# Kernel optimization log

Measured on AMD Instinct MI355X. Metric: run time of the kernel, lower is better.

Reference implementation:

```python
import jax, jax.numpy as jnp
import numpy as np

R, C = 30, 56
N = R * C  # 1680
K = 0.005
PRCN = 15
ALPHA = 1.0
BETA = 1.0


def setup_inputs() -> dict:
    key = jax.random.key(0)
    k1, k2 = jax.random.split(key)
    net_in = jax.random.normal(k1, (2 * N,), dtype=jnp.float32)
    # Recurrent connectivity matrix (learned weight in the original, loaded from .mat)
    J = jax.random.normal(k2, (N, N), dtype=jnp.float32) / np.float32(np.sqrt(N))
    return {"net_in": net_in, "J": J}


def reference(net_in, J):
    Iext = net_in[:N].reshape(R, C)
    r0 = net_in[N:2 * N].reshape(R, C)

    def step(r, _):
        # 4-way chunked mm + cat in the original == single matvec J @ r_flat
        temp = (J @ r.reshape(N)).reshape(R, C)
        U = ALPHA * (BETA * temp) + ALPHA * Iext
        sq = jnp.square(0.2 * U)
        recSum = jnp.sum(K * sq)
        # (0.2*U)^2 * (0.04 / recSum) / 0.04  ==  sq / recSum, kept explicit for fidelity
        r_new = sq * (0.04 / recSum) / 0.04
        return r_new, (U, recSum)

    r_last, (Us, sums) = jax.lax.scan(step, r0, None, length=PRCN - 1)
    return Us[-1], sums[-1], r_last
```

## Files before the change

### kernel.cpp

```cpp
#include <hip/hip_runtime.h>


typedef float f32x4 __attribute__((ext_vector_type(4)));

#define N      1680
#define NV4    420
#define NSTEP  14
#define GBLK   105
#define RPB    16
#define RPW    4

__device__ __forceinline__ void jload7_issue(
    const f32x4* p0, const f32x4* p1, const f32x4* p2, const f32x4* p3,
    const f32x4* p4, const f32x4* p5, const f32x4* p6,
    f32x4& v0, f32x4& v1, f32x4& v2, f32x4& v3,
    f32x4& v4, f32x4& v5, f32x4& v6)
{
    asm volatile(
        "global_load_dwordx4 %0, %7, off\n\t"
        "global_load_dwordx4 %1, %8, off\n\t"
        "global_load_dwordx4 %2, %9, off\n\t"
        "global_load_dwordx4 %3, %10, off\n\t"
        "global_load_dwordx4 %4, %11, off\n\t"
        "global_load_dwordx4 %5, %12, off\n\t"
        "global_load_dwordx4 %6, %13, off"
        : "=&v"(v0), "=&v"(v1), "=&v"(v2), "=&v"(v3),
          "=&v"(v4), "=&v"(v5), "=&v"(v6)
        : "v"(p0), "v"(p1), "v"(p2), "v"(p3), "v"(p4), "v"(p5), "v"(p6));
}

__device__ __forceinline__ void vm_wait0() {
    asm volatile("s_waitcnt vmcnt(0)" ::: "memory");
    __builtin_amdgcn_sched_barrier(0);
}

__device__ __forceinline__ void load7_llc(
    const f32x4* p0, const f32x4* p1, const f32x4* p2, const f32x4* p3,
    const f32x4* p4, const f32x4* p5, const f32x4* p6,
    f32x4& v0, f32x4& v1, f32x4& v2, f32x4& v3,
    f32x4& v4, f32x4& v5, f32x4& v6)
{
    asm volatile(
        "global_load_dwordx4 %0, %7, off sc0 sc1\n\t"
        "global_load_dwordx4 %1, %8, off sc0 sc1\n\t"
        "global_load_dwordx4 %2, %9, off sc0 sc1\n\t"
        "global_load_dwordx4 %3, %10, off sc0 sc1\n\t"
        "global_load_dwordx4 %4, %11, off sc0 sc1\n\t"
        "global_load_dwordx4 %5, %12, off sc0 sc1\n\t"
        "global_load_dwordx4 %6, %13, off sc0 sc1\n\t"
        "s_waitcnt vmcnt(0)"
        : "=&v"(v0), "=&v"(v1), "=&v"(v2), "=&v"(v3),
          "=&v"(v4), "=&v"(v5), "=&v"(v6)
        : "v"(p0), "v"(p1), "v"(p2), "v"(p3), "v"(p4), "v"(p5), "v"(p6)
        : "memory");
}

__device__ __forceinline__ void llc_store4(f32x4* p, f32x4 v) {
    asm volatile("global_store_dwordx4 %0, %1, off sc0 sc1"
                 :: "v"(p), "v"(v) : "memory");
}

__global__ __launch_bounds__(256, 1) void fused_recur(
    const float* __restrict__ J,
    const float* __restrict__ net_in,
    float* __restrict__ out,
    float* __restrict__ ws)
{
    __shared__ f32x4 lds_r[2][NV4];
    __shared__ float lds_flag[16];

    f32x4* bufs = (f32x4*)ws;

    const int tid  = threadIdx.x;
    const int lane = tid & 63;
    const int wave = tid >> 6;
    const int row0 = (int)blockIdx.x * RPB + wave * RPW;

    const unsigned pend0 = (lane < 36) ? 0x7Fu : 0x3Fu;

    if (tid < 16) lds_flag[tid] = 0.0f;
    __syncthreads();

    float iext[RPW];
    #pragma unroll
    for (int m = 0; m < RPW; ++m) iext[m] = net_in[row0 + m];

    const f32x4* jb[RPW];
    #pragma unroll
    for (int m = 0; m < RPW; ++m)
        jb[m] = (const f32x4*)(J + (size_t)(row0 + m) * N);

    float Uv[RPW], Qv[RPW];

    #pragma unroll 1
    for (int t = 0; t < NSTEP; ++t) {
        f32x4 Jr[RPW][7];
        #pragma unroll
        for (int m = 0; m < RPW; ++m)
            jload7_issue(jb[m] + lane,       jb[m] + lane + 64,
                         jb[m] + lane + 128, jb[m] + lane + 192,
                         jb[m] + lane + 256, jb[m] + lane + 320,
                         (lane < 36) ? (jb[m] + lane + 384) : jb[m],
                         Jr[m][0], Jr[m][1], Jr[m][2], Jr[m][3],
                         Jr[m][4], Jr[m][5], Jr[m][6]);

        f32x4 rv[7];
        float psum = 0.0f;
        const int par = (t - 1) & 1;

        if (t == 0) {
            vm_wait0();
            const f32x4* r0 = (const f32x4*)(net_in + N);
            #pragma unroll
            for (int k = 0; k < 7; ++k) {
                const int idx = lane + 64 * k;
                rv[k] = (idx < NV4) ? r0[idx] : (f32x4)0.f;
            }
        } else if (wave == 0) {
            const f32x4* base = bufs + (size_t)(t - 1) * NV4;
            const f32x4* q0 = base + lane;
            const f32x4* q1 = base + lane + 64;
            const f32x4* q2 = base + lane + 128;
            const f32x4* q3 = base + lane + 192;
            const f32x4* q4 = base + lane + 256;
            const f32x4* q5 = base + lane + 320;
            const f32x4* q6 = (lane < 36) ? (base + lane + 384) : base;

            unsigned pend = pend0;
            #pragma unroll 1
            for (;;) {
                load7_llc(q0, q1, q2, q3, q4, q5, q6,
                          rv[0], rv[1], rv[2], rv[3], rv[4], rv[5], rv[6]);
                #pragma unroll
                for (int k = 0; k < 7; ++k) {
                    if ((pend >> k) & 1u) {
                        const f32x4 q = rv[k];
                        const float mn = fminf(fminf(q[0], q[1]),
                                               fminf(q[2], q[3]));
                        if (mn >= 0.0f) {
                            lds_r[par][lane + 64 * k] = q;
                            pend &= ~(1u << k);
                        }
                    }
                }
                if (!__any(pend != 0u)) break;
            }
            if (lane == 0)
                __hip_atomic_store(&lds_flag[t - 1], 1.0f, __ATOMIC_RELEASE,
                                   __HIP_MEMORY_SCOPE_WORKGROUP);
            if (lane >= 36) rv[6] = (f32x4)0.f;
            #pragma unroll
            for (int k = 0; k < 7; ++k)
                psum += (rv[k][0] + rv[k][1]) + (rv[k][2] + rv[k][3]);
        } else {
            while (__hip_atomic_load(&lds_flag[t - 1], __ATOMIC_ACQUIRE,
                                     __HIP_MEMORY_SCOPE_WORKGROUP) == 0.0f) {}
            vm_wait0();
            #pragma unroll
            for (int k = 0; k < 7; ++k) {
                const int idx = lane + 64 * k;
                rv[k] = (idx < NV4) ? lds_r[par][idx] : (f32x4)0.f;
            }
            #pragma unroll
            for (int k = 0; k < 7; ++k)
                psum += (rv[k][0] + rv[k][1]) + (rv[k][2] + rv[k][3]);
        }

        f32x4 acc[RPW];
        #pragma unroll
        for (int m = 0; m < RPW; ++m) acc[m] = (f32x4)0.f;
        #pragma unroll
        for (int k = 0; k < 7; ++k) {
            #pragma unroll
            for (int m = 0; m < RPW; ++m) {
                acc[m][0] += Jr[m][k][0] * rv[k][0];
                acc[m][1] += Jr[m][k][1] * rv[k][1];
                acc[m][2] += Jr[m][k][2] * rv[k][2];
                acc[m][3] += Jr[m][k][3] * rv[k][3];
            }
        }
        float red[5];
        #pragma unroll
        for (int m = 0; m < RPW; ++m)
            red[m] = (acc[m][0] + acc[m][1]) + (acc[m][2] + acc[m][3]);
        red[4] = psum;
        #pragma unroll
        for (int off = 32; off; off >>= 1) {
            #pragma unroll
            for (int i = 0; i < 5; ++i) red[i] += __shfl_xor(red[i], off, 64);
        }
        const float inv = (t == 0) ? 1.0f : 1.0f / (0.005f * red[4]);

        #pragma unroll
        for (int m = 0; m < RPW; ++m) {
            const float U  = red[m] * inv + iext[m];
            const float u2 = 0.2f * U;
            Uv[m] = U;
            Qv[m] = u2 * u2;
        }

        if (lane == 0) {
            f32x4 pub = { Qv[0], Qv[1], Qv[2], Qv[3] };
            llc_store4(bufs + (size_t)t * NV4 + (row0 >> 2), pub);
        }
    }

    float s13;
    if (wave == 0) {
        const f32x4* base = bufs + (size_t)(NSTEP - 1) * NV4;
        const f32x4* q0 = base + lane;
        const f32x4* q1 = base + lane + 64;
        const f32x4* q2 = base + lane + 128;
        const f32x4* q3 = base + lane + 192;
        const f32x4* q4 = base + lane + 256;
        const f32x4* q5 = base + lane + 320;
        const f32x4* q6 = (lane < 36) ? (base + lane + 384) : base;
        f32x4 rv[7];
        unsigned pend = pend0;
        float psum = 0.0f;
        #pragma unroll 1
        for (;;) {
            load7_llc(q0, q1, q2, q3, q4, q5, q6,
                      rv[0], rv[1], rv[2], rv[3], rv[4], rv[5], rv[6]);
            #pragma unroll
            for (int k = 0; k < 7; ++k) {
                if ((pend >> k) & 1u) {
                    const f32x4 q = rv[k];
                    const float mn = fminf(fminf(q[0], q[1]), fminf(q[2], q[3]));
                    if (mn >= 0.0f) {
                        psum += (q[0] + q[1]) + (q[2] + q[3]);
                        pend &= ~(1u << k);
                    }
                }
            }
            if (!__any(pend != 0u)) break;
        }
        #pragma unroll
        for (int off = 32; off; off >>= 1) psum += __shfl_xor(psum, off, 64);
        s13 = 0.005f * psum;
        if (lane == 0)
            __hip_atomic_store(&lds_flag[15], s13, __ATOMIC_RELEASE,
                               __HIP_MEMORY_SCOPE_WORKGROUP);
    } else {
        float f;
        while ((f = __hip_atomic_load(&lds_flag[15], __ATOMIC_ACQUIRE,
                                      __HIP_MEMORY_SCOPE_WORKGROUP)) == 0.0f) {}
        s13 = f;
    }

    if (lane == 0) {
        f32x4 u4 = { Uv[0], Uv[1], Uv[2], Uv[3] };
        *(f32x4*)(out + row0) = u4;
    }
    if (lane < RPW) {
        const float q = (lane == 0) ? Qv[0] : (lane == 1) ? Qv[1]
                       : (lane == 2) ? Qv[2] : Qv[3];
        out[N + 1 + row0 + lane] = q / s13;
    }
    if (blockIdx.x == 0 && tid == 0) out[N] = s13;
}

extern "C" void kernel_launch(void* const* d_in, const int* in_sizes, int n_in,
                              void* d_out, int out_size, void* d_ws, size_t ws_size,
                              hipStream_t stream) {
    const float* net_in = (const float*)d_in[0];
    const float* J      = (const float*)d_in[1];
    hipMemsetAsync(d_ws, 0xBF, (size_t)NSTEP * NV4 * sizeof(f32x4), stream);
    fused_recur<<<GBLK, 256, 0, stream>>>(J, net_in, (float*)d_out, (float*)d_ws);
}
```

Before: 111.3 us.

## Dedicate a fifth wave to polling and staging the global state vector

Adds a dedicated producer wave per block that polls the LLC-published r vector for each step and copies it into double-buffered LDS, signalling the compute waves through LDS flags. The four compute waves now only load J, read r from LDS, and publish their rows, so the polling latency is taken off the compute wave 0 critical path. The final sum is also computed by every compute wave from LDS instead of a separate poll. The cost is an extra wave per block and reliance on the double buffer not being overwritten before slower compute waves read it.

```diff
diff --git a/kernel.cpp b/kernel.cpp
--- a/kernel.cpp
+++ b/kernel.cpp
@@ -60,7 +60,7 @@
                  :: "v"(p), "v"(v) : "memory");
 }
 
-__global__ __launch_bounds__(256, 1) void fused_recur(
+__global__ __launch_bounds__(320, 1) void fused_recur(
     const float* __restrict__ J,
     const float* __restrict__ net_in,
     float* __restrict__ out,
@@ -74,50 +74,16 @@
     const int tid  = threadIdx.x;
     const int lane = tid & 63;
     const int wave = tid >> 6;
-    const int row0 = (int)blockIdx.x * RPB + wave * RPW;
 
     const unsigned pend0 = (lane < 36) ? 0x7Fu : 0x3Fu;
 
     if (tid < 16) lds_flag[tid] = 0.0f;
     __syncthreads();
 
-    float iext[RPW];
-    #pragma unroll
-    for (int m = 0; m < RPW; ++m) iext[m] = net_in[row0 + m];
-
-    const f32x4* jb[RPW];
-    #pragma unroll
-    for (int m = 0; m < RPW; ++m)
-        jb[m] = (const f32x4*)(J + (size_t)(row0 + m) * N);
-
-    float Uv[RPW], Qv[RPW];
-
-    #pragma unroll 1
-    for (int t = 0; t < NSTEP; ++t) {
-        f32x4 Jr[RPW][7];
-        #pragma unroll
-        for (int m = 0; m < RPW; ++m)
-            jload7_issue(jb[m] + lane,       jb[m] + lane + 64,
-                         jb[m] + lane + 128, jb[m] + lane + 192,
-                         jb[m] + lane + 256, jb[m] + lane + 320,
-                         (lane < 36) ? (jb[m] + lane + 384) : jb[m],
-                         Jr[m][0], Jr[m][1], Jr[m][2], Jr[m][3],
-                         Jr[m][4], Jr[m][5], Jr[m][6]);
-
-        f32x4 rv[7];
-        float psum = 0.0f;
-        const int par = (t - 1) & 1;
-
-        if (t == 0) {
-            vm_wait0();
-            const f32x4* r0 = (const f32x4*)(net_in + N);
-            #pragma unroll
-            for (int k = 0; k < 7; ++k) {
-                const int idx = lane + 64 * k;
-                rv[k] = (idx < NV4) ? r0[idx] : (f32x4)0.f;
-            }
-        } else if (wave == 0) {
-            const f32x4* base = bufs + (size_t)(t - 1) * NV4;
+    if (wave == 0) {
+        #pragma unroll 1
+        for (int t = 0; t < NSTEP; ++t) {
+            const f32x4* base = bufs + (size_t)t * NV4;
             const f32x4* q0 = base + lane;
             const f32x4* q1 = base + lane + 64;
             const f32x4* q2 = base + lane + 128;
@@ -125,10 +91,12 @@
             const f32x4* q4 = base + lane + 256;
             const f32x4* q5 = base + lane + 320;
             const f32x4* q6 = (lane < 36) ? (base + lane + 384) : base;
+            f32x4* dst = lds_r[t & 1];
 
             unsigned pend = pend0;
             #pragma unroll 1
             for (;;) {
+                f32x4 rv[7];
                 load7_llc(q0, q1, q2, q3, q4, q5, q6,
                           rv[0], rv[1], rv[2], rv[3], rv[4], rv[5], rv[6]);
                 #pragma unroll
@@ -138,7 +106,7 @@
                         const float mn = fminf(fminf(q[0], q[1]),
                                                fminf(q[2], q[3]));
                         if (mn >= 0.0f) {
-                            lds_r[par][lane + 64 * k] = q;
+                            dst[lane + 64 * k] = q;
                             pend &= ~(1u << k);
                         }
                     }
@@ -146,25 +114,63 @@
                 if (!__any(pend != 0u)) break;
             }
             if (lane == 0)
-                __hip_atomic_store(&lds_flag[t - 1], 1.0f, __ATOMIC_RELEASE,
+                __hip_atomic_store(&lds_flag[t], 1.0f, __ATOMIC_RELEASE,
                                    __HIP_MEMORY_SCOPE_WORKGROUP);
-            if (lane >= 36) rv[6] = (f32x4)0.f;
-            #pragma unroll
-            for (int k = 0; k < 7; ++k)
-                psum += (rv[k][0] + rv[k][1]) + (rv[k][2] + rv[k][3]);
+        }
+        return;
+    }
+
+    const int w    = wave - 1;
+    const int row0 = (int)blockIdx.x * RPB + w * RPW;
+
+    float iext[RPW];
+    #pragma unroll
+    for (int m = 0; m < RPW; ++m) iext[m] = net_in[row0 + m];
+
+    const f32x4* jb[RPW];
+    #pragma unroll
+    for (int m = 0; m < RPW; ++m)
+        jb[m] = (const f32x4*)(J + (size_t)(row0 + m) * N);
+
+    float Uv[RPW], Qv[RPW];
+
+    #pragma unroll 1
+    for (int t = 0; t < NSTEP; ++t) {
+        f32x4 Jr[RPW][7];
+        #pragma unroll
+        for (int m = 0; m < RPW; ++m)
+            jload7_issue(jb[m] + lane,       jb[m] + lane + 64,
+                         jb[m] + lane + 128, jb[m] + lane + 192,
+                         jb[m] + lane + 256, jb[m] + lane + 320,
+                         (lane < 36) ? (jb[m] + lane + 384) : jb[m],
+                         Jr[m][0], Jr[m][1], Jr[m][2], Jr[m][3],
+                         Jr[m][4], Jr[m][5], Jr[m][6]);
+
+        f32x4 rv[7];
+        float psum = 0.0f;
+
+        if (t == 0) {
+            vm_wait0();
+            const f32x4* r0 = (const f32x4*)(net_in + N);
+            #pragma unroll
+            for (int k = 0; k < 7; ++k) {
+                const int idx = lane + 64 * k;
+                rv[k] = (idx < NV4) ? r0[idx] : (f32x4)0.f;
+            }
         } else {
             while (__hip_atomic_load(&lds_flag[t - 1], __ATOMIC_ACQUIRE,
                                      __HIP_MEMORY_SCOPE_WORKGROUP) == 0.0f) {}
             vm_wait0();
+            const f32x4* src = lds_r[(t - 1) & 1];
             #pragma unroll
             for (int k = 0; k < 7; ++k) {
                 const int idx = lane + 64 * k;
-                rv[k] = (idx < NV4) ? lds_r[par][idx] : (f32x4)0.f;
-            }
-            #pragma unroll
-            for (int k = 0; k < 7; ++k)
-                psum += (rv[k][0] + rv[k][1]) + (rv[k][2] + rv[k][3]);
-        }
+                rv[k] = (idx < NV4) ? src[idx] : (f32x4)0.f;
+            }
+        }
+        #pragma unroll
+        for (int k = 0; k < 7; ++k)
+            psum += (rv[k][0] + rv[k][1]) + (rv[k][2] + rv[k][3]);
 
         f32x4 acc[RPW];
         #pragma unroll
@@ -205,48 +211,23 @@
         }
     }
 
-    float s13;
-    if (wave == 0) {
-        const f32x4* base = bufs + (size_t)(NSTEP - 1) * NV4;
-        const f32x4* q0 = base + lane;
-        const f32x4* q1 = base + lane + 64;
-        const f32x4* q2 = base + lane + 128;
-        const f32x4* q3 = base + lane + 192;
-        const f32x4* q4 = base + lane + 256;
-        const f32x4* q5 = base + lane + 320;
-        const f32x4* q6 = (lane < 36) ? (base + lane + 384) : base;
-        f32x4 rv[7];
-        unsigned pend = pend0;
-        float psum = 0.0f;
-        #pragma unroll 1
-        for (;;) {
-            load7_llc(q0, q1, q2, q3, q4, q5, q6,
-                      rv[0], rv[1], rv[2], rv[3], rv[4], rv[5], rv[6]);
-            #pragma unroll
-            for (int k = 0; k < 7; ++k) {
-                if ((pend >> k) & 1u) {
-                    const f32x4 q = rv[k];
-                    const float mn = fminf(fminf(q[0], q[1]), fminf(q[2], q[3]));
-                    if (mn >= 0.0f) {
-                        psum += (q[0] + q[1]) + (q[2] + q[3]);
-                        pend &= ~(1u << k);
-                    }
-                }
-            }
-            if (!__any(pend != 0u)) break;
-        }
-        #pragma unroll
-        for (int off = 32; off; off >>= 1) psum += __shfl_xor(psum, off, 64);
-        s13 = 0.005f * psum;
-        if (lane == 0)
-            __hip_atomic_store(&lds_flag[15], s13, __ATOMIC_RELEASE,
-                               __HIP_MEMORY_SCOPE_WORKGROUP);
-    } else {
-        float f;
-        while ((f = __hip_atomic_load(&lds_flag[15], __ATOMIC_ACQUIRE,
-                                      __HIP_MEMORY_SCOPE_WORKGROUP)) == 0.0f) {}
-        s13 = f;
-    }
+    while (__hip_atomic_load(&lds_flag[NSTEP - 1], __ATOMIC_ACQUIRE,
+                             __HIP_MEMORY_SCOPE_WORKGROUP) == 0.0f) {}
+    float psum = 0.0f;
+    {
+        const f32x4* src = lds_r[(NSTEP - 1) & 1];
+        #pragma unroll
+        for (int k = 0; k < 7; ++k) {
+            const int idx = lane + 64 * k;
+            if (idx < NV4) {
+                const f32x4 q = src[idx];
+                psum += (q[0] + q[1]) + (q[2] + q[3]);
+            }
+        }
+    }
+    #pragma unroll
+    for (int off = 32; off; off >>= 1) psum += __shfl_xor(psum, off, 64);
+    const float s13 = 0.005f * psum;
 
     if (lane == 0) {
         f32x4 u4 = { Uv[0], Uv[1], Uv[2], Uv[3] };
@@ -257,7 +238,7 @@
                        : (lane == 2) ? Qv[2] : Qv[3];
         out[N + 1 + row0 + lane] = q / s13;
     }
-    if (blockIdx.x == 0 && tid == 0) out[N] = s13;
+    if (blockIdx.x == 0 && tid == 64) out[N] = s13;
 }
 
 extern "C" void kernel_launch(void* const* d_in, const int* in_sizes, int n_in,
@@ -266,5 +247,5 @@
     const float* net_in = (const float*)d_in[0];
     const float* J      = (const float*)d_in[1];
     hipMemsetAsync(d_ws, 0xBF, (size_t)NSTEP * NV4 * sizeof(f32x4), stream);
-    fused_recur<<<GBLK, 256, 0, stream>>>(J, net_in, (float*)d_out, (float*)d_ws);
-}
+    fused_recur<<<GBLK, 320, 0, stream>>>(J, net_in, (float*)d_out, (float*)d_ws);
+}
```

After: 116.7 us. 4.9% more time.

## Double-buffer J registers and stream per-chunk flags to overlap polling with FMA

Applied to the files above, without the earlier changes.

Prefetches the next step's J rows into a second register set during the step tail, so the J loads for step t+1 overlap the wait for step t's published state. The single per-step LDS flag becomes seven per-chunk flags. The polling wave accumulates each chunk as soon as it arrives, and the other waves consume chunks incrementally instead of waiting for the whole vector. The final recSum is now computed redundantly by every wave from LDS rather than broadcast through a flag. Keeping two J register sets doubles register pressure and may cause spills, and the per-chunk __all checks add polling overhead.

```diff
diff --git a/kernel.cpp b/kernel.cpp
--- a/kernel.cpp
+++ b/kernel.cpp
@@ -67,7 +67,7 @@
     float* __restrict__ ws)
 {
     __shared__ f32x4 lds_r[2][NV4];
-    __shared__ float lds_flag[16];
+    __shared__ float lds_flag[NSTEP][8];
 
     f32x4* bufs = (f32x4*)ws;
 
@@ -78,7 +78,7 @@
 
     const unsigned pend0 = (lane < 36) ? 0x7Fu : 0x3Fu;
 
-    if (tid < 16) lds_flag[tid] = 0.0f;
+    if (tid < NSTEP * 8) ((float*)lds_flag)[tid] = 0.0f;
     __syncthreads();
 
     float iext[RPW];
@@ -90,33 +90,84 @@
     for (int m = 0; m < RPW; ++m)
         jb[m] = (const f32x4*)(J + (size_t)(row0 + m) * N);
 
+    f32x4 JA[RPW][7], JB[RPW][7];
+    #pragma unroll
+    for (int m = 0; m < RPW; ++m)
+        jload7_issue(jb[m] + lane,       jb[m] + lane + 64,
+                     jb[m] + lane + 128, jb[m] + lane + 192,
+                     jb[m] + lane + 256, jb[m] + lane + 320,
+                     (lane < 36) ? (jb[m] + lane + 384) : jb[m],
+                     JA[m][0], JA[m][1], JA[m][2], JA[m][3],
+                     JA[m][4], JA[m][5], JA[m][6]);
+
     float Uv[RPW], Qv[RPW];
 
-    #pragma unroll 1
-    for (int t = 0; t < NSTEP; ++t) {
-        f32x4 Jr[RPW][7];
+    auto step_tail = [&](int t, float red[5], f32x4 (&Jnxt)[RPW][7]) {
+        #pragma unroll
+        for (int off = 32; off; off >>= 1) {
+            #pragma unroll
+            for (int i = 0; i < 5; ++i) red[i] += __shfl_xor(red[i], off, 64);
+        }
+        const float inv = (t == 0) ? 1.0f : 1.0f / (0.005f * red[4]);
+        #pragma unroll
+        for (int m = 0; m < RPW; ++m) {
+            const float U  = red[m] * inv + iext[m];
+            const float u2 = 0.2f * U;
+            Uv[m] = U;
+            Qv[m] = u2 * u2;
+        }
+        if (lane == 0) {
+            f32x4 pub = { Qv[0], Qv[1], Qv[2], Qv[3] };
+            llc_store4(bufs + (size_t)t * NV4 + (row0 >> 2), pub);
+        }
+        if (t + 1 < NSTEP) {
+            #pragma unroll
+            for (int m = 0; m < RPW; ++m)
+                jload7_issue(jb[m] + lane,       jb[m] + lane + 64,
+                             jb[m] + lane + 128, jb[m] + lane + 192,
+                             jb[m] + lane + 256, jb[m] + lane + 320,
+                             (lane < 36) ? (jb[m] + lane + 384) : jb[m],
+                             Jnxt[m][0], Jnxt[m][1], Jnxt[m][2], Jnxt[m][3],
+                             Jnxt[m][4], Jnxt[m][5], Jnxt[m][6]);
+        }
+    };
+
+    {
+        vm_wait0();
+        const f32x4* r0 = (const f32x4*)(net_in + N);
+        f32x4 acc[RPW];
+        #pragma unroll
+        for (int m = 0; m < RPW; ++m) acc[m] = (f32x4)0.f;
+        float psum = 0.0f;
+        #pragma unroll
+        for (int k = 0; k < 7; ++k) {
+            const int idx = lane + 64 * k;
+            const f32x4 q = (idx < NV4) ? r0[idx] : (f32x4)0.f;
+            #pragma unroll
+            for (int m = 0; m < RPW; ++m) {
+                acc[m][0] += JA[m][k][0] * q[0];
+                acc[m][1] += JA[m][k][1] * q[1];
+                acc[m][2] += JA[m][k][2] * q[2];
+                acc[m][3] += JA[m][k][3] * q[3];
+            }
+            psum += (q[0] + q[1]) + (q[2] + q[3]);
+        }
+        float red[5];
         #pragma unroll
         for (int m = 0; m < RPW; ++m)
-            jload7_issue(jb[m] + lane,       jb[m] + lane + 64,
-                         jb[m] + lane + 128, jb[m] + lane + 192,
-                         jb[m] + lane + 256, jb[m] + lane + 320,
-                         (lane < 36) ? (jb[m] + lane + 384) : jb[m],
-                         Jr[m][0], Jr[m][1], Jr[m][2], Jr[m][3],
-                         Jr[m][4], Jr[m][5], Jr[m][6]);
-
-        f32x4 rv[7];
+            red[m] = (acc[m][0] + acc[m][1]) + (acc[m][2] + acc[m][3]);
+        red[4] = psum;
+        step_tail(0, red, JB);
+    }
+
+    auto step_body = [&](int t, f32x4 (&Jcur)[RPW][7], f32x4 (&Jnxt)[RPW][7]) {
+        const int par = (t - 1) & 1;
+        f32x4 acc[RPW];
+        #pragma unroll
+        for (int m = 0; m < RPW; ++m) acc[m] = (f32x4)0.f;
         float psum = 0.0f;
-        const int par = (t - 1) & 1;
-
-        if (t == 0) {
-            vm_wait0();
-            const f32x4* r0 = (const f32x4*)(net_in + N);
-            #pragma unroll
-            for (int k = 0; k < 7; ++k) {
-                const int idx = lane + 64 * k;
-                rv[k] = (idx < NV4) ? r0[idx] : (f32x4)0.f;
-            }
-        } else if (wave == 0) {
+
+        if (wave == 0) {
             const f32x4* base = bufs + (size_t)(t - 1) * NV4;
             const f32x4* q0 = base + lane;
             const f32x4* q1 = base + lane + 64;
@@ -126,9 +177,10 @@
             const f32x4* q5 = base + lane + 320;
             const f32x4* q6 = (lane < 36) ? (base + lane + 384) : base;
 
-            unsigned pend = pend0;
+            unsigned pend = pend0, fleft = 0x7Fu;
             #pragma unroll 1
             for (;;) {
+                f32x4 rv[7];
                 load7_llc(q0, q1, q2, q3, q4, q5, q6,
                           rv[0], rv[1], rv[2], rv[3], rv[4], rv[5], rv[6]);
                 #pragma unroll
@@ -139,113 +191,126 @@
                                                fminf(q[2], q[3]));
                         if (mn >= 0.0f) {
                             lds_r[par][lane + 64 * k] = q;
+                            #pragma unroll
+                            for (int m = 0; m < RPW; ++m) {
+                                acc[m][0] += Jcur[m][k][0] * q[0];
+                                acc[m][1] += Jcur[m][k][1] * q[1];
+                                acc[m][2] += Jcur[m][k][2] * q[2];
+                                acc[m][3] += Jcur[m][k][3] * q[3];
+                            }
+                            psum += (q[0] + q[1]) + (q[2] + q[3]);
                             pend &= ~(1u << k);
                         }
                     }
                 }
+                #pragma unroll
+                for (int k = 0; k < 7; ++k) {
+                    if ((fleft >> k) & 1u) {
+                        if (__all(((pend >> k) & 1u) == 0u)) {
+                            if (lane == 0)
+                                __hip_atomic_store(&lds_flag[t - 1][k], 1.0f,
+                                                   __ATOMIC_RELEASE,
+                                                   __HIP_MEMORY_SCOPE_WORKGROUP);
+                            fleft &= ~(1u << k);
+                        }
+                    }
+                }
                 if (!__any(pend != 0u)) break;
             }
-            if (lane == 0)
-                __hip_atomic_store(&lds_flag[t - 1], 1.0f, __ATOMIC_RELEASE,
-                                   __HIP_MEMORY_SCOPE_WORKGROUP);
-            if (lane >= 36) rv[6] = (f32x4)0.f;
-            #pragma unroll
-            for (int k = 0; k < 7; ++k)
-                psum += (rv[k][0] + rv[k][1]) + (rv[k][2] + rv[k][3]);
         } else {
-            while (__hip_atomic_load(&lds_flag[t - 1], __ATOMIC_ACQUIRE,
-                                     __HIP_MEMORY_SCOPE_WORKGROUP) == 0.0f) {}
-            vm_wait0();
             #pragma unroll
             for (int k = 0; k < 7; ++k) {
-                const int idx = lane + 64 * k;
-                rv[k] = (idx < NV4) ? lds_r[par][idx] : (f32x4)0.f;
-            }
-            #pragma unroll
-            for (int k = 0; k < 7; ++k)
-                psum += (rv[k][0] + rv[k][1]) + (rv[k][2] + rv[k][3]);
-        }
-
-        f32x4 acc[RPW];
-        #pragma unroll
-        for (int m = 0; m < RPW; ++m) acc[m] = (f32x4)0.f;
-        #pragma unroll
-        for (int k = 0; k < 7; ++k) {
-            #pragma unroll
-            for (int m = 0; m < RPW; ++m) {
-                acc[m][0] += Jr[m][k][0] * rv[k][0];
-                acc[m][1] += Jr[m][k][1] * rv[k][1];
-                acc[m][2] += Jr[m][k][2] * rv[k][2];
-                acc[m][3] += Jr[m][k][3] * rv[k][3];
-            }
-        }
+                while (__hip_atomic_load(&lds_flag[t - 1][k], __ATOMIC_ACQUIRE,
+                                         __HIP_MEMORY_SCOPE_WORKGROUP) == 0.0f) {}
+                if (k == 0) vm_wait0();
+                if (k < 6 || lane < 36) {
+                    const f32x4 q = lds_r[par][lane + 64 * k];
+                    #pragma unroll
+                    for (int m = 0; m < RPW; ++m) {
+                        acc[m][0] += Jcur[m][k][0] * q[0];
+                        acc[m][1] += Jcur[m][k][1] * q[1];
+                        acc[m][2] += Jcur[m][k][2] * q[2];
+                        acc[m][3] += Jcur[m][k][3] * q[3];
+                    }
+                    psum += (q[0] + q[1]) + (q[2] + q[3]);
+                }
+            }
+        }
+
         float red[5];
         #pragma unroll
         for (int m = 0; m < RPW; ++m)
             red[m] = (acc[m][0] + acc[m][1]) + (acc[m][2] + acc[m][3]);
         red[4] = psum;
-        #pragma unroll
-        for (int off = 32; off; off >>= 1) {
-            #pragma unroll
-            for (int i = 0; i < 5; ++i) red[i] += __shfl_xor(red[i], off, 64);
-        }
-        const float inv = (t == 0) ? 1.0f : 1.0f / (0.005f * red[4]);
-
-        #pragma unroll
-        for (int m = 0; m < RPW; ++m) {
-            const float U  = red[m] * inv + iext[m];
-            const float u2 = 0.2f * U;
-            Uv[m] = U;
-            Qv[m] = u2 * u2;
-        }
-
-        if (lane == 0) {
-            f32x4 pub = { Qv[0], Qv[1], Qv[2], Qv[3] };
-            llc_store4(bufs + (size_t)t * NV4 + (row0 >> 2), pub);
-        }
+        step_tail(t, red, Jnxt);
+    };
+
+    #pragma unroll 1
+    for (int tt = 1; tt < NSTEP; tt += 2) {
+        step_body(tt, JB, JA);
+        if (tt + 1 < NSTEP) step_body(tt + 1, JA, JB);
     }
 
     float s13;
-    if (wave == 0) {
-        const f32x4* base = bufs + (size_t)(NSTEP - 1) * NV4;
-        const f32x4* q0 = base + lane;
-        const f32x4* q1 = base + lane + 64;
-        const f32x4* q2 = base + lane + 128;
-        const f32x4* q3 = base + lane + 192;
-        const f32x4* q4 = base + lane + 256;
-        const f32x4* q5 = base + lane + 320;
-        const f32x4* q6 = (lane < 36) ? (base + lane + 384) : base;
-        f32x4 rv[7];
-        unsigned pend = pend0;
+    {
         float psum = 0.0f;
-        #pragma unroll 1
-        for (;;) {
-            load7_llc(q0, q1, q2, q3, q4, q5, q6,
-                      rv[0], rv[1], rv[2], rv[3], rv[4], rv[5], rv[6]);
+        if (wave == 0) {
+            const f32x4* base = bufs + (size_t)(NSTEP - 1) * NV4;
+            const f32x4* q0 = base + lane;
+            const f32x4* q1 = base + lane + 64;
+            const f32x4* q2 = base + lane + 128;
+            const f32x4* q3 = base + lane + 192;
+            const f32x4* q4 = base + lane + 256;
+            const f32x4* q5 = base + lane + 320;
+            const f32x4* q6 = (lane < 36) ? (base + lane + 384) : base;
+            unsigned pend = pend0, fleft = 0x7Fu;
+            #pragma unroll 1
+            for (;;) {
+                f32x4 rv[7];
+                load7_llc(q0, q1, q2, q3, q4, q5, q6,
+                          rv[0], rv[1], rv[2], rv[3], rv[4], rv[5], rv[6]);
+                #pragma unroll
+                for (int k = 0; k < 7; ++k) {
+                    if ((pend >> k) & 1u) {
+                        const f32x4 q = rv[k];
+                        const float mn = fminf(fminf(q[0], q[1]),
+                                               fminf(q[2], q[3]));
+                        if (mn >= 0.0f) {
+                            lds_r[1][lane + 64 * k] = q;
+                            psum += (q[0] + q[1]) + (q[2] + q[3]);
+                            pend &= ~(1u << k);
+                        }
+                    }
+                }
+                #pragma unroll
+                for (int k = 0; k < 7; ++k) {
+                    if ((fleft >> k) & 1u) {
+                        if (__all(((pend >> k) & 1u) == 0u)) {
+                            if (lane == 0)
+                                __hip_atomic_store(&lds_flag[NSTEP - 1][k], 1.0f,
+                                                   __ATOMIC_RELEASE,
+                                                   __HIP_MEMORY_SCOPE_WORKGROUP);
+                            fleft &= ~(1u << k);
+                        }
+                    }
+                }
+                if (!__any(pend != 0u)) break;
+            }
+        } else {
             #pragma unroll
             for (int k = 0; k < 7; ++k) {
-                if ((pend >> k) & 1u) {
-                    const f32x4 q = rv[k];
-                    const float mn = fminf(fminf(q[0], q[1]), fminf(q[2], q[3]));
-                    if (mn >= 0.0f) {
-                        psum += (q[0] + q[1]) + (q[2] + q[3]);
-                        pend &= ~(1u << k);
-                    }
-                }
-            }
-            if (!__any(pend != 0u)) break;
+                while (__hip_atomic_load(&lds_flag[NSTEP - 1][k],
+                                         __ATOMIC_ACQUIRE,
+                                         __HIP_MEMORY_SCOPE_WORKGROUP) == 0.0f) {}
+                if (k < 6 || lane < 36) {
+                    const f32x4 q = lds_r[1][lane + 64 * k];
+                    psum += (q[0] + q[1]) + (q[2] + q[3]);
+                }
+            }
         }
         #pragma unroll
         for (int off = 32; off; off >>= 1) psum += __shfl_xor(psum, off, 64);
         s13 = 0.005f * psum;
-        if (lane == 0)
-            __hip_atomic_store(&lds_flag[15], s13, __ATOMIC_RELEASE,
-                               __HIP_MEMORY_SCOPE_WORKGROUP);
-    } else {
-        float f;
-        while ((f = __hip_atomic_load(&lds_flag[15], __ATOMIC_ACQUIRE,
-                                      __HIP_MEMORY_SCOPE_WORKGROUP)) == 0.0f) {}
-        s13 = f;
     }
 
     if (lane == 0) {
```

After: 119.3 us. 1.07x slower.
